# Kernel optimization log

Hardware: AMD Instinct MI355X
Metric: run time of the kernel (lower is better)

The kernel has to match this reference:

```python
import jax, jax.numpy as jnp
import numpy as np

B, T, D, I, E, R = 4, 2048, 2048, 6144, 8, 32


def setup_inputs() -> dict:
    key = jax.random.key(0)
    ks = jax.random.split(key, 9)
    return {
        "x": jax.random.normal(ks[0], (B, T, D), jnp.float32),
        "router_w": jax.random.normal(ks[1], (D, E), jnp.float32) * 0.02,
        "A_gate": jax.random.normal(ks[2], (E, D, R), jnp.float32) * 0.01,
        "B_gate": jax.random.normal(ks[3], (E, R, I), jnp.float32) * 0.01,
        "A_up": jax.random.normal(ks[4], (E, D, R), jnp.float32) * 0.01,
        "B_up": jax.random.normal(ks[5], (E, R, I), jnp.float32) * 0.01,
        "W_gate": jax.random.normal(ks[6], (D, I), jnp.float32) * 0.02,
        "W_up": jax.random.normal(ks[7], (D, I), jnp.float32) * 0.02,
        "W_down": jax.random.normal(ks[8], (I, D), jnp.float32) * 0.02,
    }


def reference(x, router_w, A_gate, B_gate, A_up, B_up, W_gate, W_up, W_down):
    b, t, d = x.shape
    flat = x.reshape(b * t, d)                     # [N, D]
    # Router: top-1 expert per token (argmax matches torch argmax: first max)
    gate_logits = flat @ router_w                  # [N, E]
    idx = jnp.argmax(gate_logits, axis=-1)         # [N]
    n_exp = router_w.shape[1]

    def routed_lora(A, Bm):
        # sum_e mask_e * (x @ A_e @ B_e); loop over small static expert count
        out = jnp.zeros((flat.shape[0], Bm.shape[2]), flat.dtype)
        for e in range(n_exp):
            m = (idx == e)[:, None]
            out = out + jnp.where(m, (flat @ A[e]) @ Bm[e], 0.0)
        return out

    # ExpertLoRA forward: base gate/up + per-token-selected LoRA delta, SwiGLU, down
    gate = flat @ W_gate + routed_lora(A_gate, B_gate)   # [N, I]
    up = flat @ W_up + routed_lora(A_up, B_up)           # [N, I]
    down = (jax.nn.silu(gate) * up) @ W_down             # [N, D]
    return down.reshape(b, t, d), gate_logits
```

## Files before the change

kernel.cpp:

```cpp
#include <hip/hip_runtime.h>
#include <stdint.h>

#define N_TOK 8192
#define DDIM 2048
#define IDIM 6144
#define NEXP 8
#define RLORA 32
#define NCHUNK 64
#define CHUNK 128

typedef __attribute__((ext_vector_type(8))) short short8;
typedef __attribute__((ext_vector_type(4))) float floatx4;
typedef __attribute__((ext_vector_type(4))) unsigned short ushortx4;

__device__ __forceinline__ unsigned short f2bf(float f) {
  union { float f; unsigned u; } v; v.f = f;
  unsigned u = v.u;
  unsigned r = (u + 0x7fffu + ((u >> 16) & 1u)) >> 16;
  return (unsigned short)r;
}

__device__ __forceinline__ void gload_lds16(const void* g, void* l) {
  __builtin_amdgcn_global_load_lds(
      (const __attribute__((address_space(1))) void*)g,
      (__attribute__((address_space(3))) void*)l, 16, 0, 0);
}

__global__ __launch_bounds__(256) void router_kernel(
    const float* __restrict__ x, const float* __restrict__ rw,
    float* __restrict__ logits_out, int* __restrict__ idx) {
  int wave = threadIdx.x >> 6, lane = threadIdx.x & 63;
  int n = blockIdx.x * 4 + wave;
  const float* xr = x + (size_t)n * DDIM;
  float acc[NEXP];
#pragma unroll
  for (int e = 0; e < NEXP; e++) acc[e] = 0.f;
#pragma unroll
  for (int j = 0; j < 8; j++) {
    int d = j * 256 + lane * 4;
    floatx4 v = *(const floatx4*)(xr + d);
    const float* rwd = rw + (size_t)d * NEXP;
#pragma unroll
    for (int t = 0; t < 4; t++) {
      float xv = v[t];
      const float* rr = rwd + t * NEXP;
#pragma unroll
      for (int e = 0; e < NEXP; e++) acc[e] += xv * rr[e];
    }
  }
#pragma unroll
  for (int off = 32; off > 0; off >>= 1) {
#pragma unroll
    for (int e = 0; e < NEXP; e++) acc[e] += __shfl_xor(acc[e], off, 64);
  }
  if (lane == 0) {
    float best = acc[0]; int bi = 0;
#pragma unroll
    for (int e = 1; e < NEXP; e++)
      if (acc[e] > best) { best = acc[e]; bi = e; }
    idx[n] = bi;
#pragma unroll
    for (int e = 0; e < NEXP; e++) logits_out[(size_t)n * NEXP + e] = acc[e];
  }
}

__global__ __launch_bounds__(128) void count_kernel(
    const int* __restrict__ idx, int* __restrict__ cnt) {
  __shared__ int h[NEXP];
  if (threadIdx.x < NEXP) h[threadIdx.x] = 0;
  __syncthreads();
  int n = blockIdx.x * CHUNK + threadIdx.x;
  atomicAdd(&h[idx[n]], 1);
  __syncthreads();
  if (threadIdx.x < NEXP) cnt[blockIdx.x * NEXP + threadIdx.x] = h[threadIdx.x];
}

__global__ __launch_bounds__(64) void scan_kernel(
    const int* __restrict__ cnt, int* __restrict__ off) {
  __shared__ int tot[NEXP], base[NEXP];
  int t = threadIdx.x;
  if (t < NEXP) {
    int s = 0;
    for (int c = 0; c < NCHUNK; c++) s += cnt[c * NEXP + t];
    tot[t] = s;
  }
  __syncthreads();
  if (t == 0) {
    int run = 0;
    for (int e = 0; e < NEXP; e++) { base[e] = run; run += tot[e]; }
  }
  __syncthreads();
  if (t < NEXP) {
    int run = base[t];
    for (int c = 0; c < NCHUNK; c++) { off[c * NEXP + t] = run; run += cnt[c * NEXP + t]; }
  }
}

__global__ __launch_bounds__(64) void rank_kernel(
    const int* __restrict__ idx, const int* __restrict__ off,
    int* __restrict__ sortpos, int* __restrict__ orig, int* __restrict__ eidx) {
  if (threadIdx.x != 0) return;
  int c = blockIdx.x;
  int lc[NEXP];
#pragma unroll
  for (int e = 0; e < NEXP; e++) lc[e] = 0;
  for (int t = 0; t < CHUNK; t++) {
    int n = c * CHUNK + t;
    int e = idx[n];
    int dst = off[c * NEXP + e] + lc[e]++;
    sortpos[n] = dst;
    orig[dst] = n;
    eidx[dst] = e;
  }
}

__global__ __launch_bounds__(256) void permute_x_kernel(
    const float* __restrict__ x, const int* __restrict__ sortpos,
    unsigned short* __restrict__ xb) {
  int wave = threadIdx.x >> 6, lane = threadIdx.x & 63;
  int n = blockIdx.x * 4 + wave;
  int dst = sortpos[n];
  const float* xr = x + (size_t)n * DDIM;
  unsigned short* xbr = xb + (size_t)dst * DDIM;
#pragma unroll
  for (int j = 0; j < 8; j++) {
    int d = j * 256 + lane * 4;
    floatx4 v = *(const floatx4*)(xr + d);
    ushortx4 s;
    s[0] = f2bf(v[0]); s[1] = f2bf(v[1]); s[2] = f2bf(v[2]); s[3] = f2bf(v[3]);
    *(ushortx4*)(xbr + d) = s;
  }
}

__global__ __launch_bounds__(256) void transpose_w_kernel(
    const float* __restrict__ in, unsigned short* __restrict__ out, int Rr, int Cc) {
  __shared__ float lds[32][33];
  int r0 = blockIdx.y * 32, c0 = blockIdx.x * 32;
  int tx = threadIdx.x & 31, ty = threadIdx.x >> 5;
#pragma unroll
  for (int k = 0; k < 4; k++) {
    int r = ty + k * 8;
    lds[r][tx] = in[(size_t)(r0 + r) * Cc + c0 + tx];
  }
  __syncthreads();
#pragma unroll
  for (int k = 0; k < 4; k++) {
    int cc = ty + k * 8;
    out[(size_t)(c0 + cc) * Rr + r0 + tx] = f2bf(lds[tx][cc]);
  }
}

__global__ __launch_bounds__(256) void transpose_wint_kernel(
    const float* __restrict__ Wg, const float* __restrict__ Wu,
    unsigned short* __restrict__ wint) {
  __shared__ float lds[32][33];
  int r0 = blockIdx.y * 32, c0 = blockIdx.x * 32;
  const float* in = blockIdx.z ? Wu : Wg;
  int w = blockIdx.z;
  int tx = threadIdx.x & 31, ty = threadIdx.x >> 5;
#pragma unroll
  for (int k = 0; k < 4; k++) {
    int r = ty + k * 8;
    lds[r][tx] = in[(size_t)(r0 + r) * IDIM + c0 + tx];
  }
  __syncthreads();
#pragma unroll
  for (int k = 0; k < 4; k++) {
    int cc = ty + k * 8;
    wint[(size_t)(2 * (c0 + cc) + w) * DDIM + r0 + tx] = f2bf(lds[tx][cc]);
  }
}

__global__ __launch_bounds__(256) void pack_a_kernel(
    const float* __restrict__ Ag, const float* __restrict__ Au,
    unsigned short* __restrict__ aat) {
  int o = blockIdx.x * 256 + threadIdx.x;
  int h = o >> 19;
  int oo = o & ((1 << 19) - 1);
  int c = oo >> 11, d = oo & 2047;
  int e = c >> 5, r = c & 31;
  const float* src = h ? Au : Ag;
  float v = src[(e << 16) + (d << 5) + r];
  aat[(size_t)(h * 256 + c) * DDIM + d] = f2bf(v);
}

__global__ __launch_bounds__(256) void pack_bl_kernel(
    const float* __restrict__ Bg, const float* __restrict__ Bu,
    unsigned short* __restrict__ BL) {
  int o = (blockIdx.x * 256 + threadIdx.x) * 4;
  int kk = o & 63;
  int t2 = o >> 6;
  int c = t2 % (2 * IDIM);
  int e = t2 / (2 * IDIM);
  int j = c >> 1, w = c & 1;
  ushortx4 s;
#pragma unroll
  for (int r = 0; r < 4; r++) {
    int k = kk + r;
    float v;
    if (w == 0) v = (k < 32) ? Bg[((size_t)e * RLORA + k) * IDIM + j] : 0.f;
    else        v = (k >= 32) ? Bu[((size_t)e * RLORA + (k - 32)) * IDIM + j] : 0.f;
    s[r] = f2bf(v);
  }
  *(ushortx4*)(BL + o) = s;
}

__global__ __launch_bounds__(256) void gemm_tsel_kernel(
    const unsigned short* __restrict__ xb, const unsigned short* __restrict__ aat,
    const int* __restrict__ eidx, unsigned short* __restrict__ Tsel) {
  __shared__ __align__(16) unsigned short sA[4096], sB[2048];
  __shared__ int es_s[128];
  const int row0 = blockIdx.x * 128;
  const int tid = threadIdx.x;
  const int wave = tid >> 6, lane = tid & 63;
  const int wr = wave >> 1, wc = wave & 1;
  const int q = lane >> 4, m16 = lane & 15;
  if (tid < 128) es_s[tid] = eidx[row0 + tid];
  __syncthreads();
  const int emin = es_s[0], emax = es_s[127];
  int erow[4];
#pragma unroll
  for (int m = 0; m < 4; m++) erow[m] = es_s[wr * 64 + m * 16 + m16];
  floatx4 acc[8];
#pragma unroll
  for (int i = 0; i < 8; i++)
#pragma unroll
    for (int j = 0; j < 4; j++) acc[i][j] = 0.f;
  short8 zero;
#pragma unroll
  for (int i = 0; i < 8; i++) zero[i] = 0;
  for (int ee = emin; ee <= emax; ee++) {
    for (int k0 = 0; k0 < DDIM; k0 += 32) {
      __syncthreads();
#pragma unroll
      for (int rr = 0; rr < 2; rr++) {
        int e = tid * 8 + rr * 2048;
        int r = e >> 5, kk = e & 31;
        gload_lds16(xb + (size_t)(row0 + r) * DDIM + (k0 + kk), sA + e);
      }
      {
        int e2 = tid * 8;
        int c = e2 >> 5, kk = e2 & 31;
        int srow = (c < 32) ? (ee * 32 + c) : (256 + ee * 32 + (c - 32));
        gload_lds16(aat + (size_t)srow * DDIM + (k0 + kk), sB + e2);
      }
      __syncthreads();
      short8 a[4], b[2];
#pragma unroll
      for (int m = 0; m < 4; m++) {
        short8 av = *(const short8*)(sA + (wr * 64 + m * 16 + m16) * 32 + q * 8);
        a[m] = (erow[m] == ee) ? av : zero;
      }
#pragma unroll
      for (int n = 0; n < 2; n++)
        b[n] = *(const short8*)(sB + (wc * 32 + n * 16 + m16) * 32 + q * 8);
#pragma unroll
      for (int m = 0; m < 4; m++)
#pragma unroll
        for (int n = 0; n < 2; n++)
          acc[m * 2 + n] = __builtin_amdgcn_mfma_f32_16x16x32_bf16(a[m], b[n], acc[m * 2 + n], 0, 0, 0);
    }
  }
#pragma unroll
  for (int m = 0; m < 4; m++)
#pragma unroll
    for (int n = 0; n < 2; n++)
#pragma unroll
      for (int r = 0; r < 4; r++) {
        int grow = row0 + wr * 64 + m * 16 + q * 4 + r;
        int gcol = wc * 32 + n * 16 + m16;
        Tsel[(size_t)grow * 64 + gcol] = f2bf(acc[m * 2 + n][r]);
      }
}

__device__ __forceinline__ void mm256_main(const unsigned short* __restrict__ Aptr,
                                           const unsigned short* __restrict__ Bptr,
                                           int K, int row0, int col0,
                                           unsigned short* smem, floatx4* acc) {
  const int tid = threadIdx.x;
  const int lane = tid & 63, wave = tid >> 6;
  const int wm = wave >> 2, wn = wave & 3;
  const int q = lane >> 4, m16 = lane & 15;
  const int NT = K >> 5;

  int offA[8], offB[4];
#pragma unroll
  for (int m = 0; m < 8; m++) {
    int rw2 = wm * 128 + m * 16 + m16;
    offA[m] = rw2 * 32 + ((q ^ ((rw2 >> 1) & 3)) * 8);
  }
#pragma unroll
  for (int n = 0; n < 4; n++) {
    int c = wn * 64 + n * 16 + m16;
    offB[n] = 8192 + c * 32 + ((q ^ ((c >> 1) & 3)) * 8);
  }

  auto stageA = [&](int kt) {
    unsigned short* Ab = smem + (kt & 3) * 16384;
#pragma unroll
    for (int ch = 0; ch < 2; ch++) {
      int o = ch * 4096 + tid * 8;
      int rw2 = o >> 5, g = (o >> 3) & 3;
      int gs = g ^ ((rw2 >> 1) & 3);
      gload_lds16(Aptr + (size_t)(row0 + rw2) * K + kt * 32 + gs * 8, Ab + o);
    }
  };
  auto stageB = [&](int kt) {
    unsigned short* Bb = smem + (kt & 3) * 16384 + 8192;
#pragma unroll
    for (int ch = 0; ch < 2; ch++) {
      int o = ch * 4096 + tid * 8;
      int rw2 = o >> 5, g = (o >> 3) & 3;
      int gs = g ^ ((rw2 >> 1) & 3);
      gload_lds16(Bptr + (size_t)(col0 + rw2) * K + kt * 32 + gs * 8, Bb + o);
    }
  };

  stageA(0); stageB(0); stageA(1); stageB(1); stageA(2); stageB(2);
  asm volatile("s_waitcnt vmcnt(8)" ::: "memory");
  __builtin_amdgcn_s_barrier();
  __builtin_amdgcn_sched_barrier(0);

  for (int kt = 0; kt < NT; kt++) {
    const unsigned short* base = smem + (kt & 3) * 16384;
    short8 a[8], b[4];
#pragma unroll
    for (int m = 0; m < 4; m++) a[m] = *(const short8*)(base + offA[m]);
#pragma unroll
    for (int n = 0; n < 4; n++) b[n] = *(const short8*)(base + offB[n]);
    __builtin_amdgcn_sched_barrier(0);
#pragma unroll
    for (int m = 4; m < 8; m++) a[m] = *(const short8*)(base + offA[m]);
    if (kt + 3 < NT) { stageA(kt + 3); stageB(kt + 3); }
    asm volatile("s_waitcnt lgkmcnt(4)" ::: "memory");
    __builtin_amdgcn_sched_barrier(0);
    __builtin_amdgcn_s_setprio(1);
#pragma unroll
    for (int m = 0; m < 4; m++)
#pragma unroll
      for (int n = 0; n < 4; n++)
        acc[m * 4 + n] = __builtin_amdgcn_mfma_f32_16x16x32_bf16(a[m], b[n], acc[m * 4 + n], 0, 0, 0);
    asm volatile("s_waitcnt lgkmcnt(0)" ::: "memory");
    __builtin_amdgcn_sched_barrier(0);
#pragma unroll
    for (int m = 4; m < 8; m++)
#pragma unroll
      for (int n = 0; n < 4; n++)
        acc[16 + (m - 4) * 4 + n] = __builtin_amdgcn_mfma_f32_16x16x32_bf16(a[m], b[n], acc[16 + (m - 4) * 4 + n], 0, 0, 0);
    __builtin_amdgcn_s_setprio(0);
    if (kt < NT - 3)       asm volatile("s_waitcnt vmcnt(8)" ::: "memory");
    else if (kt == NT - 3) asm volatile("s_waitcnt vmcnt(4)" ::: "memory");
    else if (kt == NT - 2) asm volatile("s_waitcnt vmcnt(0)" ::: "memory");
    __builtin_amdgcn_s_barrier();
  }
}

__global__ __launch_bounds__(512, 2) void gemm_gateup_kernel(
    const unsigned short* __restrict__ xb, const unsigned short* __restrict__ wint,
    const unsigned short* __restrict__ Tsel, const unsigned short* __restrict__ BL,
    const int* __restrict__ eidx, unsigned short* __restrict__ hbuf) {
  __shared__ __align__(16) unsigned short smem[65536];

  int lin = blockIdx.x;
  int xcd = lin & 7, slot = lin >> 3;
  int grp = slot >> 6, r = slot & 63;
  int bx = xcd * 6 + grp * 2 + (r & 1);
  int by = r >> 1;
  const int row0 = by * 256, col0 = bx * 256;

  const int tid = threadIdx.x;
  const int lane = tid & 63, wave = tid >> 6;
  const int wm = wave >> 2, wn = wave & 3;
  const int q = lane >> 4, m16 = lane & 15;

  floatx4 acc[32];
#pragma unroll
  for (int i = 0; i < 32; i++)
#pragma unroll
    for (int j = 0; j < 4; j++) acc[i][j] = 0.f;

  mm256_main(xb, wint, DDIM, row0, col0, smem, acc);

#pragma unroll
  for (int ch = 0; ch < 4; ch++) {
    int o = ch * 4096 + tid * 8;
    int rw2 = o >> 6, g = (o >> 3) & 7;
    int gs = g ^ (rw2 & 7);
    gload_lds16(Tsel + (size_t)(row0 + rw2) * 64 + gs * 8, smem + o);
  }
  int* es = (int*)(smem + 32768);
  if (tid < 64) gload_lds16(eidx + row0 + tid * 4, (void*)(es + tid * 4));
  asm volatile("s_waitcnt vmcnt(0)" ::: "memory");
  __builtin_amdgcn_s_barrier();
  __builtin_amdgcn_sched_barrier(0);

  const int emin = es[0], emax = es[255];
  int erow[8];
#pragma unroll
  for (int m = 0; m < 8; m++) erow[m] = es[wm * 128 + m * 16 + m16];

  auto stage_bl = [&](int ee) {
#pragma unroll
    for (int ch = 0; ch < 4; ch++) {
      int o = ch * 4096 + tid * 8;
      int c = o >> 6, g = (o >> 3) & 7;
      int gs = g ^ (c & 7);
      gload_lds16(BL + ((size_t)ee * (2 * IDIM) + col0 + c) * 64 + gs * 8, smem + 16384 + o);
    }
  };
  stage_bl(emin);
  asm volatile("s_waitcnt vmcnt(0)" ::: "memory");
  __builtin_amdgcn_s_barrier();
  __builtin_amdgcn_sched_barrier(0);

  short8 zero;
#pragma unroll
  for (int i = 0; i < 8; i++) zero[i] = 0;

  for (int ee = emin; ee <= emax; ee++) {
    short8 bl[4][2];
#pragma unroll
    for (int n = 0; n < 4; n++) {
      int c = wn * 64 + n * 16 + m16;
#pragma unroll
      for (int kk = 0; kk < 2; kk++) {
        int gg = (kk * 4 + q) ^ (c & 7);
        bl[n][kk] = *(const short8*)(smem + 16384 + c * 64 + gg * 8);
      }
    }
#pragma unroll
    for (int m = 0; m < 8; m++) {
      int rw2 = wm * 128 + m * 16 + m16;
      short8 tgm[2];
#pragma unroll
      for (int kk = 0; kk < 2; kk++) {
        int gg = (kk * 4 + q) ^ (rw2 & 7);
        short8 v = *(const short8*)(smem + rw2 * 64 + gg * 8);
        tgm[kk] = (erow[m] == ee) ? v : zero;
      }
#pragma unroll
      for (int n = 0; n < 4; n++)
#pragma unroll
        for (int kk = 0; kk < 2; kk++)
          acc[m * 4 + n] = __builtin_amdgcn_mfma_f32_16x16x32_bf16(tgm[kk], bl[n][kk], acc[m * 4 + n], 0, 0, 0);
    }
    if (ee < emax) {
      __builtin_amdgcn_s_barrier();
      stage_bl(ee + 1);
      asm volatile("s_waitcnt vmcnt(0)" ::: "memory");
      __builtin_amdgcn_s_barrier();
      __builtin_amdgcn_sched_barrier(0);
    }
  }

#pragma unroll
  for (int m = 0; m < 8; m++)
#pragma unroll
    for (int n = 0; n < 4; n++)
#pragma unroll
      for (int rr2 = 0; rr2 < 4; rr2++) {
        float v = acc[m * 4 + n][rr2];
        float p = __shfl_xor(v, 1, 64);
        float g = (m16 & 1) ? p : v;
        float u = (m16 & 1) ? v : p;
        float h = g / (1.f + __expf(-g)) * u;
        if (!(m16 & 1)) {
          int grow = row0 + wm * 128 + m * 16 + q * 4 + rr2;
          int gi = (col0 + wn * 64 + n * 16 + m16) >> 1;
          hbuf[(size_t)grow * IDIM + gi] = f2bf(h);
        }
      }
}

__global__ __launch_bounds__(512, 2) void gemm_down_kernel(
    const unsigned short* __restrict__ hb, const unsigned short* __restrict__ wdt,
    const int* __restrict__ orig, float* __restrict__ out) {
  __shared__ __align__(16) unsigned short smem[65536];
  int lin = blockIdx.x;
  int bx = lin & 7, by = lin >> 3;
  const int row0 = by * 256, col0 = bx * 256;

  floatx4 acc[32];
#pragma unroll
  for (int i = 0; i < 32; i++)
#pragma unroll
    for (int j = 0; j < 4; j++) acc[i][j] = 0.f;

  mm256_main(hb, wdt, IDIM, row0, col0, smem, acc);

  const int tid = threadIdx.x;
  const int lane = tid & 63, wave = tid >> 6;
  const int wm = wave >> 2, wn = wave & 3;
  const int q = lane >> 4, m16 = lane & 15;
#pragma unroll
  for (int m = 0; m < 8; m++)
#pragma unroll
    for (int n = 0; n < 4; n++)
#pragma unroll
      for (int r = 0; r < 4; r++) {
        int grow = row0 + wm * 128 + m * 16 + q * 4 + r;
        int orow = orig[grow];
        int gcol = col0 + wn * 64 + n * 16 + m16;
        out[(size_t)orow * DDIM + gcol] = acc[m * 4 + n][r];
      }
}

extern "C" void kernel_launch(void* const* d_in, const int* in_sizes, int n_in,
                              void* d_out, int out_size, void* d_ws, size_t ws_size,
                              hipStream_t stream) {
  const float* x  = (const float*)d_in[0];
  const float* rw = (const float*)d_in[1];
  const float* Ag = (const float*)d_in[2];
  const float* Bg = (const float*)d_in[3];
  const float* Au = (const float*)d_in[4];
  const float* Bu = (const float*)d_in[5];
  const float* Wg = (const float*)d_in[6];
  const float* Wu = (const float*)d_in[7];
  const float* Wd = (const float*)d_in[8];
  float* out = (float*)d_out;
  float* logits = out + (size_t)N_TOK * DDIM;

  char* ws = (char*)d_ws;
  size_t off = 0;
  auto alloc = [&](size_t bytes) {
    char* p = ws + off;
    off += (bytes + 255) & ~(size_t)255;
    return p;
  };
  unsigned short* xb  = (unsigned short*)alloc((size_t)N_TOK * DDIM * 2);
  unsigned short* wint= (unsigned short*)alloc((size_t)2 * IDIM * DDIM * 2);
  unsigned short* wdt = (unsigned short*)alloc((size_t)DDIM * IDIM * 2);
  unsigned short* aat = (unsigned short*)alloc((size_t)512 * DDIM * 2);
  unsigned short* BL  = (unsigned short*)alloc((size_t)NEXP * 2 * IDIM * 64 * 2);
  unsigned short* Tsel= (unsigned short*)alloc((size_t)N_TOK * 64 * 2);
  unsigned short* hbuf= (unsigned short*)alloc((size_t)N_TOK * IDIM * 2);
  int* idx     = (int*)alloc((size_t)N_TOK * 4);
  int* sortpos = (int*)alloc((size_t)N_TOK * 4);
  int* orig    = (int*)alloc((size_t)N_TOK * 4);
  int* eidx    = (int*)alloc((size_t)N_TOK * 4);
  int* cnt     = (int*)alloc((size_t)NCHUNK * NEXP * 4);
  int* offb    = (int*)alloc((size_t)NCHUNK * NEXP * 4);

  router_kernel<<<N_TOK / 4, 256, 0, stream>>>(x, rw, logits, idx);
  count_kernel<<<NCHUNK, 128, 0, stream>>>(idx, cnt);
  scan_kernel<<<1, 64, 0, stream>>>(cnt, offb);
  rank_kernel<<<NCHUNK, 64, 0, stream>>>(idx, offb, sortpos, orig, eidx);
  permute_x_kernel<<<N_TOK / 4, 256, 0, stream>>>(x, sortpos, xb);
  transpose_w_kernel<<<dim3(DDIM / 32, IDIM / 32), 256, 0, stream>>>(Wd, wdt, IDIM, DDIM);
  transpose_wint_kernel<<<dim3(IDIM / 32, DDIM / 32, 2), 256, 0, stream>>>(Wg, Wu, wint);
  pack_a_kernel<<<4096, 256, 0, stream>>>(Ag, Au, aat);
  pack_bl_kernel<<<(NEXP * 2 * IDIM * 64) / 1024, 256, 0, stream>>>(Bg, Bu, BL);
  gemm_tsel_kernel<<<N_TOK / 128, 256, 0, stream>>>(xb, aat, eidx, Tsel);
  gemm_gateup_kernel<<<(N_TOK / 256) * (2 * IDIM / 256), 512, 0, stream>>>(
      xb, wint, Tsel, BL, eidx, hbuf);
  gemm_down_kernel<<<256, 512, 0, stream>>>(hbuf, wdt, orig, out);
}
```

Before: 1.028 ms.

## Software-pipeline MFMA second half across k-tiles with double-buffered B fragments

Restructures the gate/up GEMM main loop so the second half of each k-tile's MFMAs (rows 4-7) runs at the start of the next iteration, overlapping the LDS fragment reads for the next tile. B fragments are ping-ponged between two register sets and the loop is unrolled by two, with a prologue and epilogue. This hides LDS read latency behind matrix work, at the cost of more live registers, which could pressure occupancy at 512 threads with 2 blocks per CU.

```diff
diff --git a/kernel.cpp b/kernel.cpp
--- a/kernel.cpp
+++ b/kernel.cpp
@@ -316,22 +316,59 @@
     }
   };
 
+  short8 aX[4], aY[4], bE[4], bO[4];
+
+#define GU_BODY(KT, BN, BP)                                                    \
+  {                                                                            \
+    const unsigned short* base = smem + ((KT) & 3) * 16384;                    \
+    __builtin_amdgcn_s_setprio(1);                                             \
+    _Pragma("unroll")                                                          \
+    for (int m = 0; m < 4; m++)                                                \
+      _Pragma("unroll")                                                        \
+      for (int n = 0; n < 4; n++)                                              \
+        acc[16 + m * 4 + n] = __builtin_amdgcn_mfma_f32_16x16x32_bf16(         \
+            aY[m], BP[n], acc[16 + m * 4 + n], 0, 0, 0);                       \
+    __builtin_amdgcn_s_setprio(0);                                             \
+    _Pragma("unroll")                                                          \
+    for (int m = 0; m < 4; m++) aX[m] = *(const short8*)(base + offA[m]);      \
+    _Pragma("unroll")                                                          \
+    for (int n = 0; n < 4; n++) BN[n] = *(const short8*)(base + offB[n]);      \
+    __builtin_amdgcn_sched_barrier(0);                                         \
+    _Pragma("unroll")                                                          \
+    for (int m = 0; m < 4; m++) aY[m] = *(const short8*)(base + offA[4 + m]);  \
+    if ((KT) + 3 < NT) { stageA((KT) + 3); stageB((KT) + 3); }                 \
+    asm volatile("s_waitcnt lgkmcnt(4)" ::: "memory");                         \
+    __builtin_amdgcn_sched_barrier(0);                                         \
+    __builtin_amdgcn_s_setprio(1);                                             \
+    _Pragma("unroll")                                                          \
+    for (int m = 0; m < 4; m++)                                                \
+      _Pragma("unroll")                                                        \
+      for (int n = 0; n < 4; n++)                                              \
+        acc[m * 4 + n] = __builtin_amdgcn_mfma_f32_16x16x32_bf16(              \
+            aX[m], BN[n], acc[m * 4 + n], 0, 0, 0);                            \
+    __builtin_amdgcn_s_setprio(0);                                             \
+    asm volatile("s_waitcnt lgkmcnt(0)" ::: "memory");                         \
+    __builtin_amdgcn_sched_barrier(0);                                         \
+    if ((KT) < NT - 3)       asm volatile("s_waitcnt vmcnt(8)" ::: "memory");  \
+    else if ((KT) == NT - 3) asm volatile("s_waitcnt vmcnt(4)" ::: "memory");  \
+    else if ((KT) == NT - 2) asm volatile("s_waitcnt vmcnt(0)" ::: "memory");  \
+    __builtin_amdgcn_s_barrier();                                              \
+  }
+
   stageA(0); stageB(0); stageA(1); stageB(1); stageA(2); stageB(2);
   asm volatile("s_waitcnt vmcnt(8)" ::: "memory");
   __builtin_amdgcn_s_barrier();
   __builtin_amdgcn_sched_barrier(0);
-
-  for (int kt = 0; kt < NT; kt++) {
-    const unsigned short* base = smem + (kt & 3) * 16384;
-    short8 a[8], b[4];
-#pragma unroll
-    for (int m = 0; m < 4; m++) a[m] = *(const short8*)(base + offA[m]);
-#pragma unroll
-    for (int n = 0; n < 4; n++) b[n] = *(const short8*)(base + offB[n]);
+  {
+    const unsigned short* base = smem;
+#pragma unroll
+    for (int m = 0; m < 4; m++) aX[m] = *(const short8*)(base + offA[m]);
+#pragma unroll
+    for (int n = 0; n < 4; n++) bE[n] = *(const short8*)(base + offB[n]);
     __builtin_amdgcn_sched_barrier(0);
 #pragma unroll
-    for (int m = 4; m < 8; m++) a[m] = *(const short8*)(base + offA[m]);
-    if (kt + 3 < NT) { stageA(kt + 3); stageB(kt + 3); }
+    for (int m = 0; m < 4; m++) aY[m] = *(const short8*)(base + offA[4 + m]);
+    stageA(3); stageB(3);
     asm volatile("s_waitcnt lgkmcnt(4)" ::: "memory");
     __builtin_amdgcn_sched_barrier(0);
     __builtin_amdgcn_s_setprio(1);
@@ -339,20 +376,26 @@
     for (int m = 0; m < 4; m++)
 #pragma unroll
       for (int n = 0; n < 4; n++)
-        acc[m * 4 + n] = __builtin_amdgcn_mfma_f32_16x16x32_bf16(a[m], b[n], acc[m * 4 + n], 0, 0, 0);
+        acc[m * 4 + n] = __builtin_amdgcn_mfma_f32_16x16x32_bf16(aX[m], bE[n], acc[m * 4 + n], 0, 0, 0);
+    __builtin_amdgcn_s_setprio(0);
     asm volatile("s_waitcnt lgkmcnt(0)" ::: "memory");
     __builtin_amdgcn_sched_barrier(0);
-#pragma unroll
-    for (int m = 4; m < 8; m++)
-#pragma unroll
-      for (int n = 0; n < 4; n++)
-        acc[16 + (m - 4) * 4 + n] = __builtin_amdgcn_mfma_f32_16x16x32_bf16(a[m], b[n], acc[16 + (m - 4) * 4 + n], 0, 0, 0);
-    __builtin_amdgcn_s_setprio(0);
-    if (kt < NT - 3)       asm volatile("s_waitcnt vmcnt(8)" ::: "memory");
-    else if (kt == NT - 3) asm volatile("s_waitcnt vmcnt(4)" ::: "memory");
-    else if (kt == NT - 2) asm volatile("s_waitcnt vmcnt(0)" ::: "memory");
+    asm volatile("s_waitcnt vmcnt(8)" ::: "memory");
     __builtin_amdgcn_s_barrier();
   }
+  for (int kt = 1; kt + 1 < NT; kt += 2) {
+    GU_BODY(kt, bO, bE);
+    GU_BODY(kt + 1, bE, bO);
+  }
+  GU_BODY(NT - 1, bO, bE);
+  __builtin_amdgcn_s_setprio(1);
+#pragma unroll
+  for (int m = 0; m < 4; m++)
+#pragma unroll
+    for (int n = 0; n < 4; n++)
+      acc[16 + m * 4 + n] = __builtin_amdgcn_mfma_f32_16x16x32_bf16(aY[m], bO[n], acc[16 + m * 4 + n], 0, 0, 0);
+  __builtin_amdgcn_s_setprio(0);
+#undef GU_BODY
 }
 
 __global__ __launch_bounds__(512, 2) void gemm_gateup_kernel(
```

Result: no change. 1.028 ms (+0.0%).
